# Performance work log

Measured on AMD Instinct MI355X. Metric: run time of the kernel, lower is better.

## Reference

```python
import jax, jax.numpy as jnp
import numpy as np

B, T, C, D, P = 8, 512, 32, 128, 1024
EPS = 1e-5

def setup_inputs() -> dict:
    key = jax.random.key(0)
    ks = jax.random.split(key, 11)
    s = 1.0 / np.sqrt(D)
    inp = {
        'x': jax.random.normal(ks[0], (B, T, C, D), jnp.float32),
        'x_mask': jax.random.randint(ks[1], (B, T, C), 0, 2) == 1,
        'p_mask': jax.random.randint(ks[2], (B, T, C), 0, 2) == 1,
        'pos': jax.random.randint(ks[3], (B, T, C), 0, P),
        'pe': jax.random.normal(ks[4], (P, D // 2, 2), jnp.float32),  # complex rpe as [re, im]
        'imp': jax.random.randint(ks[5], (B, T), 0, C),
        'idx_c': jax.random.randint(ks[6], (B, T, C), 0, C),
        'wq_w': jax.random.normal(ks[7], (D, D), jnp.float32) * s,
        'wq_b': jnp.zeros((D,), jnp.float32),
        'wk_w': jax.random.normal(ks[8], (D, D), jnp.float32) * s,
        'wk_b': jnp.zeros((D,), jnp.float32),
        'wv_w': jax.random.normal(ks[9], (D, D), jnp.float32) * s,
        'wv_b': jnp.zeros((D,), jnp.float32),
        'ls_gamma': 1e-5 * jnp.ones((D,), jnp.float32),
        'ln_gamma': jnp.ones((D,), jnp.float32),
        'ln_beta': jnp.zeros((D,), jnp.float32),
    }
    return inp


def _rotate(z, r):
    # z: (b,t,c,d) real; r: (b,t,c,d/2,2) complex multiplier [re,im]
    b, t, c, d = z.shape
    zr = z.reshape(b, t, c, d // 2, 2)
    re = zr[..., 0] * r[..., 0] - zr[..., 1] * r[..., 1]
    im = zr[..., 0] * r[..., 1] + zr[..., 1] * r[..., 0]
    return jnp.stack([re, im], axis=-1).reshape(b, t, c, d)


def reference(x, x_mask, p_mask, pos, pe, imp, idx_c,
              wq_w, wq_b, wk_w, wk_b, wv_w, wv_b,
              ls_gamma, ln_gamma, ln_beta):
    b, t, c, d = x.shape
    # channel selection gather: where x_mask, use per-token important channel
    imp_rep = jnp.broadcast_to(imp[:, :, None], (b, t, c))
    idx = jnp.where(x_mask, imp_rep, idx_c)            # (b,t,c)
    xg = jnp.take_along_axis(x, idx[..., None], axis=2)  # (b,t,c,d)
    # QKV projections (torch Linear: x @ W.T + b)
    q = xg @ wq_w.T + wq_b
    k = xg @ wk_w.T + wk_b
    v = xg @ wv_w.T + wv_b
    # relative PE complex rotation on q,k
    r = pe[pos]                                        # (b,t,c,d/2,2)
    q = _rotate(q, r)
    k = _rotate(k, r)
    # (b,c,t,d) layout; channel acts as head
    qt = q.transpose(0, 2, 1, 3)
    kt = k.transpose(0, 2, 1, 3)
    vt = v.transpose(0, 2, 1, 3)
    scores = jnp.einsum('bcqd,bckd->bcqk', qt, kt) / jnp.sqrt(jnp.float32(d))
    pm = p_mask.transpose(0, 2, 1)                     # (b,c,t)
    mask = pm[:, :, :, None] | pm[:, :, None, :]       # (b,c,t,t)
    attn = jax.nn.softmax(jnp.where(mask, -jnp.inf, scores), axis=-1)
    attn = jnp.nan_to_num(attn)
    xm = x_mask.transpose(0, 2, 1)                     # (b,c,t)
    weight = jnp.where(xm, 1.0 / t, 1.0)
    out = jnp.einsum('bcmn,bcnd->bmcd', attn * weight[:, :, None, :], vt)  # (b,t,c,d)
    # norm_first=False: LN(x + layer_scale(out))
    y = x + ls_gamma * out
    mu = jnp.mean(y, axis=-1, keepdims=True)
    var = jnp.mean(jnp.square(y - mu), axis=-1, keepdims=True)
    return (y - mu) / jnp.sqrt(var + EPS) * ln_gamma + ln_beta
```

## Files before the change

kernel.cpp:

```cpp
#include <hip/hip_runtime.h>
#include <hip/hip_bf16.h>

#define Bb 8
#define Tt 512
#define Cc 32
#define Dd 128
#define SCALE 0.08838834764831845f
#define SROW 520

typedef unsigned int u32;
typedef __hip_bfloat16 bf16;
typedef __attribute__((ext_vector_type(8))) short short8;
typedef __attribute__((ext_vector_type(4))) short short4v;
typedef __attribute__((ext_vector_type(4))) float floatx4;

__device__ __forceinline__ short f2bf(float f) {
    __hip_bfloat16 h = __float2bfloat16(f);
    return *(short*)&h;
}
__device__ __forceinline__ float bf2f(short s) {
    return __uint_as_float(((u32)(unsigned short)s) << 16);
}

__global__ __launch_bounds__(256)
void k_wconv(const float* __restrict__ wq, const float* __restrict__ wk,
             const float* __restrict__ wv, short* __restrict__ Wb)
{
    int g = blockIdx.x * 256 + threadIdx.x;
    int mat = g >> 14, rem = g & 16383;
    const float* src = (mat == 0) ? wq : (mat == 1) ? wk : wv;
    Wb[g] = f2bf(src[rem]);
}

__global__ __launch_bounds__(256)
void k_qkvm(const float* __restrict__ x, const int* __restrict__ xm,
            const int* __restrict__ pos, const float* __restrict__ pe,
            const int* __restrict__ imp, const int* __restrict__ idxc,
            const short* __restrict__ Wb,
            const float* __restrict__ bq, const float* __restrict__ bk,
            const float* __restrict__ bv,
            short* __restrict__ qb, short* __restrict__ kb, short* __restrict__ vb)
{
    const int R0  = blockIdx.x * 64;
    const int b   = R0 >> 14;
    const int t0  = (R0 >> 5) & 511;
    const int tid = threadIdx.x;
    const int w    = tid >> 6;
    const int lane = tid & 63;
    const int quad = lane >> 4;
    const int m    = lane & 15;

    __shared__ short xg[64 * 136];
    __shared__ short ot[64 * 392];

#pragma unroll
    for (int i = 0; i < 8; ++i) {
        int u   = tid + i * 256;
        int row = u >> 5, seg = u & 31;
        int R   = R0 + row;
        int idx = xm[R] ? imp[R >> 5] : idxc[R];
        float4 v = *(const float4*)(x + ((long)(R >> 5) * Cc + idx) * Dd + seg * 4);
        short4v s = {f2bf(v.x), f2bf(v.y), f2bf(v.z), f2bf(v.w)};
        *(short4v*)&xg[row * 136 + seg * 4] = s;
    }

    short8 wf[6][4];
    float  bias_v[6];
#pragma unroll
    for (int mat = 0; mat < 3; ++mat) {
        const float* bp = (mat == 0) ? bq : (mat == 1) ? bk : bv;
#pragma unroll
        for (int h = 0; h < 2; ++h) {
            int sl = mat * 2 + h;
            int ct = h * 4 + w;
            bias_v[sl] = bp[ct * 16 + m];
#pragma unroll
            for (int kk = 0; kk < 4; ++kk)
                wf[sl][kk] = *(const short8*)(Wb + ((long)mat * 128 + ct * 16 + m) * 128
                                              + kk * 32 + quad * 8);
        }
    }
    __syncthreads();

    for (int rt = 0; rt < 4; ++rt) {
        short8 af[4];
#pragma unroll
        for (int kk = 0; kk < 4; ++kk)
            af[kk] = *(const short8*)&xg[(rt * 16 + m) * 136 + kk * 32 + quad * 8];

        floatx4 acc[6];
#pragma unroll
        for (int sl = 0; sl < 6; ++sl) acc[sl] = (floatx4){0.f, 0.f, 0.f, 0.f};
#pragma unroll
        for (int kk = 0; kk < 4; ++kk)
#pragma unroll
            for (int sl = 0; sl < 6; ++sl)
                acc[sl] = __builtin_amdgcn_mfma_f32_16x16x32_bf16(af[kk], wf[sl][kk], acc[sl], 0, 0, 0);

        int po[4];
#pragma unroll
        for (int r = 0; r < 4; ++r) po[r] = pos[R0 + rt * 16 + quad * 4 + r];

#pragma unroll
        for (int sl = 0; sl < 6; ++sl) {
            int mat = sl >> 1;
            int ct  = (sl & 1) * 4 + w;
            int d   = ct * 16 + m;
#pragma unroll
            for (int r = 0; r < 4; ++r) {
                float v = acc[sl][r] + bias_v[sl];
                float p = __shfl_xor(v, 1, 64);
                if (mat < 2) {
                    const float* rp = pe + ((long)po[r] * (Dd / 2) + (d >> 1)) * 2;
                    float r0 = rp[0], r1 = rp[1];
                    v = (d & 1) ? fmaf(p, r1, v * r0) : fmaf(v, r0, -(p * r1));
                    if (mat == 0) v *= SCALE;
                }
                ot[(rt * 16 + quad * 4 + r) * 392 + mat * 128 + d] = f2bf(v);
            }
        }
    }
    __syncthreads();

    short* const mats[3] = {qb, kb, vb};
#pragma unroll
    for (int mat = 0; mat < 3; ++mat) {
        short* dst = mats[mat];
#pragma unroll
        for (int i = 0; i < 4; ++i) {
            int g = tid + i * 256;
            int n = g >> 4, off = (g & 15) * 8;
            int c = n & 31, tl = n >> 5;
            *(short8*)(dst + (((long)(b * Cc + c) * Tt) + t0 + tl) * Dd + off) =
                *(const short8*)&ot[n * 392 + mat * 128 + off];
        }
    }
}

__global__ __launch_bounds__(256)
void k_vt(const short* __restrict__ vb, const int* __restrict__ xm,
          short* __restrict__ vt)
{
    const int head = blockIdx.y;
    const int b    = head >> 5;
    const int c    = head & 31;
    const int t0   = blockIdx.x * 64;
    const int tid  = threadIdx.x;

    __shared__ short tile[64 * 136];
    __shared__ float wks[64];

    if (tid < 64)
        wks[tid] = xm[((long)b * Tt + t0 + tid) * Cc + c] ? (1.0f / Tt) : 1.0f;

    const short* src = vb + ((long)head * Tt + t0) * Dd;
#pragma unroll
    for (int i = 0; i < 4; ++i) {
        int u = tid + i * 256;
        int row = u >> 4, col = (u & 15) * 8;
        *(short8*)&tile[row * 136 + col] = *(const short8*)(src + row * Dd + col);
    }
    __syncthreads();

    short* dst = vt + (long)head * Dd * Tt + t0;
#pragma unroll
    for (int i = 0; i < 4; ++i) {
        int u = tid + i * 256;
        int d = u >> 3, t8 = (u & 7) * 8;
        short8 v;
#pragma unroll
        for (int j = 0; j < 8; ++j)
            v[j] = f2bf(bf2f(tile[(t8 + j) * 136 + d]) * wks[t8 + j]);
        *(short8*)(dst + (long)d * Tt + t8) = v;
    }
}

__global__ __launch_bounds__(512, 4)
void k_attn(const short* __restrict__ qb, const short* __restrict__ kbp,
            const short* __restrict__ vtp, const float* __restrict__ x,
            const int* __restrict__ pm,
            const float* __restrict__ lsg, const float* __restrict__ lng,
            const float* __restrict__ lnb, float* __restrict__ out)
{
    const int l    = blockIdx.y * 256 + blockIdx.x;
    const int xcd  = l & 7;
    const int sws  = l >> 3;
    const int hh   = sws & 7;
    const int tl   = (sws >> 3) & 7;
    const int gg   = sws >> 6;
    const int head = xcd + ((gg * 8 + hh) << 3);
    const int b    = head >> 5;
    const int c    = head & 31;
    const int qt0  = tl * 64;
    const int tid  = threadIdx.x;
    const int w    = tid >> 6;
    const int lane = tid & 63;
    const int quad = lane >> 4;
    const int m    = lane & 15;
    const int d    = w * 16 + m;

    __shared__ short S[64 * SROW];
    __shared__ u32   pkbits[16];
    __shared__ float rlS[64];
    __shared__ float ps1[8][64];
    __shared__ float ps2[8][64];
    __shared__ float mrs[64][2];

    {
        bool v = pm[((long)b * Tt + tid) * Cc + c] != 0;
        unsigned long long bal = __ballot(v);
        if (lane == 0) {
            pkbits[w * 2]     = (u32)bal;
            pkbits[w * 2 + 1] = (u32)(bal >> 32);
        }
    }

    short8 qf[4][4];
#pragma unroll
    for (int qt = 0; qt < 4; ++qt)
#pragma unroll
        for (int kk = 0; kk < 4; ++kk)
            qf[qt][kk] = *(const short8*)(qb + ((long)head * Tt + qt0 + qt * 16 + m) * Dd
                                          + kk * 32 + quad * 8);
    __syncthreads();

    for (int ch = 0; ch < 4; ++ch) {
        int kt = ch * 128 + w * 16 + m;
        const short* kp = kbp + ((long)head * Tt + kt) * Dd + quad * 8;
        floatx4 sc[4];
#pragma unroll
        for (int qt = 0; qt < 4; ++qt) sc[qt] = (floatx4){0.f, 0.f, 0.f, 0.f};
#pragma unroll
        for (int kk = 0; kk < 4; ++kk) {
            short8 bk = *(const short8*)(kp + kk * 32);
            __builtin_amdgcn_s_setprio(1);
#pragma unroll
            for (int qt = 0; qt < 4; ++qt)
                sc[qt] = __builtin_amdgcn_mfma_f32_16x16x32_bf16(qf[qt][kk], bk, sc[qt], 0, 0, 0);
            __builtin_amdgcn_s_setprio(0);
        }
        bool masked = (pkbits[kt >> 5] >> (kt & 31)) & 1;
#pragma unroll
        for (int qt = 0; qt < 4; ++qt)
#pragma unroll
            for (int r = 0; r < 4; ++r)
                S[(qt * 16 + quad * 4 + r) * SROW + kt] = f2bf(masked ? -1e30f : sc[qt][r]);
    }

    const short* vbase = vtp + (long)head * Dd * Tt + ((long)d) * Tt + quad * 8;
    short8 bvbuf[8];
#pragma unroll
    for (int kv = 0; kv < 8; ++kv)
        bvbuf[kv] = *(const short8*)(vbase + kv * 32);

    float xv[4][4];
#pragma unroll
    for (int qt = 0; qt < 4; ++qt)
#pragma unroll
        for (int r = 0; r < 4; ++r) {
            int row = qt * 16 + quad * 4 + r;
            xv[qt][r] = x[(((long)b * Tt + qt0 + row) * Cc + c) * Dd + d];
        }
    __syncthreads();

    {
        int qi = tid >> 3, part = tid & 7;
        short* rowp = &S[qi * SROW + part * 8];
        short8 sv[8];
#pragma unroll
        for (int j = 0; j < 8; ++j) sv[j] = *(short8*)&rowp[j * 64];
        float mx = -1e30f;
#pragma unroll
        for (int j = 0; j < 8; ++j)
#pragma unroll
            for (int e = 0; e < 8; ++e) mx = fmaxf(mx, bf2f(sv[j][e]));
        mx = fmaxf(mx, __shfl_xor(mx, 1, 64));
        mx = fmaxf(mx, __shfl_xor(mx, 2, 64));
        mx = fmaxf(mx, __shfl_xor(mx, 4, 64));
        float lsum = 0.f;
#pragma unroll
        for (int j = 0; j < 8; ++j)
#pragma unroll
            for (int e = 0; e < 8; ++e) {
                float s = bf2f(sv[j][e]);
                float ex = (s <= -1e29f) ? 0.f : __expf(s - mx);
                sv[j][e] = f2bf(ex);
                lsum += ex;
            }
#pragma unroll
        for (int j = 0; j < 8; ++j) *(short8*)&rowp[j * 64] = sv[j];
        lsum += __shfl_xor(lsum, 1, 64);
        lsum += __shfl_xor(lsum, 2, 64);
        lsum += __shfl_xor(lsum, 4, 64);
        if (part == 0) {
            int t = qt0 + qi;
            bool qmask = (pkbits[t >> 5] >> (t & 31)) & 1;
            rlS[qi] = (lsum > 0.f && !qmask) ? 1.0f / lsum : 0.f;
        }
    }
    __syncthreads();

    floatx4 oa[4];
#pragma unroll
    for (int qt = 0; qt < 4; ++qt) oa[qt] = (floatx4){0.f, 0.f, 0.f, 0.f};

#pragma unroll
    for (int kv = 0; kv < 16; ++kv) {
        short8 bv = bvbuf[kv & 7];
        if (kv < 8) bvbuf[kv] = *(const short8*)(vbase + (kv + 8) * 32);
        __builtin_amdgcn_s_setprio(1);
#pragma unroll
        for (int qt = 0; qt < 4; ++qt) {
            short8 ap = *(const short8*)&S[(qt * 16 + m) * SROW + kv * 32 + quad * 8];
            oa[qt] = __builtin_amdgcn_mfma_f32_16x16x32_bf16(ap, bv, oa[qt], 0, 0, 0);
        }
        __builtin_amdgcn_s_setprio(0);
    }

    const float lg = lsg[d];
    float yv[4][4];
#pragma unroll
    for (int qt = 0; qt < 4; ++qt)
#pragma unroll
        for (int r = 0; r < 4; ++r) {
            int row = qt * 16 + quad * 4 + r;
            float val = oa[qt][r] * rlS[row];
            float y = xv[qt][r] + lg * val;
            yv[qt][r] = y;
        }
#pragma unroll
    for (int qt = 0; qt < 4; ++qt)
#pragma unroll
        for (int r = 0; r < 4; ++r) {
            float a = yv[qt][r], bb = yv[qt][r] * yv[qt][r];
            a += __shfl_xor(a, 1, 64); bb += __shfl_xor(bb, 1, 64);
            a += __shfl_xor(a, 2, 64); bb += __shfl_xor(bb, 2, 64);
            a += __shfl_xor(a, 4, 64); bb += __shfl_xor(bb, 4, 64);
            a += __shfl_xor(a, 8, 64); bb += __shfl_xor(bb, 8, 64);
            if (m == 0) {
                ps1[w][qt * 16 + quad * 4 + r] = a;
                ps2[w][qt * 16 + quad * 4 + r] = bb;
            }
        }
    __syncthreads();
    if (tid < 64) {
        float a = 0.f, bb = 0.f;
#pragma unroll
        for (int wv = 0; wv < 8; ++wv) { a += ps1[wv][tid]; bb += ps2[wv][tid]; }
        float mean = a * (1.0f / Dd);
        float var  = bb * (1.0f / Dd) - mean * mean;
        mrs[tid][0] = mean;
        mrs[tid][1] = rsqrtf(var + 1e-5f);
    }
    __syncthreads();

    const float g = lng[d], be = lnb[d];
#pragma unroll
    for (int qt = 0; qt < 4; ++qt)
#pragma unroll
        for (int r = 0; r < 4; ++r) {
            int row = qt * 16 + quad * 4 + r;
            int t = qt0 + row;
            out[(((long)b * Tt + t) * Cc + c) * Dd + d] =
                (yv[qt][r] - mrs[row][0]) * mrs[row][1] * g + be;
        }
}

extern "C" void kernel_launch(void* const* d_in, const int* in_sizes, int n_in,
                              void* d_out, int out_size, void* d_ws, size_t ws_size,
                              hipStream_t stream) {
    const float* x    = (const float*)d_in[0];
    const int* xmask  = (const int*)d_in[1];
    const int* pmask  = (const int*)d_in[2];
    const int* pos    = (const int*)d_in[3];
    const float* pe   = (const float*)d_in[4];
    const int* imp    = (const int*)d_in[5];
    const int* idxc   = (const int*)d_in[6];
    const float* wq_w = (const float*)d_in[7];
    const float* wq_b = (const float*)d_in[8];
    const float* wk_w = (const float*)d_in[9];
    const float* wk_b = (const float*)d_in[10];
    const float* wv_w = (const float*)d_in[11];
    const float* wv_b = (const float*)d_in[12];
    const float* lsg  = (const float*)d_in[13];
    const float* lng  = (const float*)d_in[14];
    const float* lnb  = (const float*)d_in[15];
    float* out = (float*)d_out;

    size_t n = (size_t)Bb * Cc * Tt * Dd;
    short* qb = (short*)d_ws;
    short* kb = qb + n;
    short* vb = kb + n;
    short* vt = vb + n;
    short* Wb = vt + n;

    k_wconv<<<dim3(3 * Dd * Dd / 256), dim3(256), 0, stream>>>(wq_w, wk_w, wv_w, Wb);
    k_qkvm<<<dim3(Bb * Tt * Cc / 64), dim3(256), 0, stream>>>(
        x, xmask, pos, pe, imp, idxc, Wb, wq_b, wk_b, wv_b, qb, kb, vb);
    k_vt<<<dim3(Tt / 64, Bb * Cc), dim3(256), 0, stream>>>(vb, xmask, vt);
    k_attn<<<dim3(256, 8), dim3(512), 0, stream>>>(
        qb, kb, vt, x, pmask, lsg, lng, lnb, out);
}
```

Before: 346.7 us.

## Swizzle V transpose LDS tile, drop V prefetch and setprio in attention

The V-transpose kernel now XOR-swizzles the 16-byte column groups of its shared tile so the transposed column reads spread across LDS banks instead of conflicting. The attention kernel drops the register-held V prefetch buffer and the early x load. It now loads V directly inside a non-unrolled PV loop and reads x after the PV matmul, and it removes the s_setprio hints. This lowers register pressure, which could help occupancy, but exposes global load latency in the PV loop and the epilogue.

```diff
diff --git a/kernel.cpp b/kernel.cpp
--- a/kernel.cpp
+++ b/kernel.cpp
@@ -157,8 +157,9 @@
 #pragma unroll
     for (int i = 0; i < 4; ++i) {
         int u = tid + i * 256;
-        int row = u >> 4, col = (u & 15) * 8;
-        *(short8*)&tile[row * 136 + col] = *(const short8*)(src + row * Dd + col);
+        int row = u >> 4, col8 = u & 15;
+        int c8 = col8 ^ ((row >> 3) & 7);
+        *(short8*)&tile[row * 136 + c8 * 8] = *(const short8*)(src + row * Dd + col8 * 8);
     }
     __syncthreads();
 
@@ -167,10 +168,12 @@
     for (int i = 0; i < 4; ++i) {
         int u = tid + i * 256;
         int d = u >> 3, t8 = (u & 7) * 8;
+        int key = u & 7;
+        int cs = ((d >> 3) ^ key) * 8 + (d & 7);
         short8 v;
 #pragma unroll
         for (int j = 0; j < 8; ++j)
-            v[j] = f2bf(bf2f(tile[(t8 + j) * 136 + d]) * wks[t8 + j]);
+            v[j] = f2bf(bf2f(tile[(t8 + j) * 136 + cs]) * wks[t8 + j]);
         *(short8*)(dst + (long)d * Tt + t8) = v;
     }
 }
@@ -197,7 +200,6 @@
     const int lane = tid & 63;
     const int quad = lane >> 4;
     const int m    = lane & 15;
-    const int d    = w * 16 + m;
 
     __shared__ short S[64 * SROW];
     __shared__ u32   pkbits[16];
@@ -233,11 +235,9 @@
 #pragma unroll
         for (int kk = 0; kk < 4; ++kk) {
             short8 bk = *(const short8*)(kp + kk * 32);
-            __builtin_amdgcn_s_setprio(1);
 #pragma unroll
             for (int qt = 0; qt < 4; ++qt)
                 sc[qt] = __builtin_amdgcn_mfma_f32_16x16x32_bf16(qf[qt][kk], bk, sc[qt], 0, 0, 0);
-            __builtin_amdgcn_s_setprio(0);
         }
         bool masked = (pkbits[kt >> 5] >> (kt & 31)) & 1;
 #pragma unroll
@@ -246,21 +246,6 @@
             for (int r = 0; r < 4; ++r)
                 S[(qt * 16 + quad * 4 + r) * SROW + kt] = f2bf(masked ? -1e30f : sc[qt][r]);
     }
-
-    const short* vbase = vtp + (long)head * Dd * Tt + ((long)d) * Tt + quad * 8;
-    short8 bvbuf[8];
-#pragma unroll
-    for (int kv = 0; kv < 8; ++kv)
-        bvbuf[kv] = *(const short8*)(vbase + kv * 32);
-
-    float xv[4][4];
-#pragma unroll
-    for (int qt = 0; qt < 4; ++qt)
-#pragma unroll
-        for (int r = 0; r < 4; ++r) {
-            int row = qt * 16 + quad * 4 + r;
-            xv[qt][r] = x[(((long)b * Tt + qt0 + row) * Cc + c) * Dd + d];
-        }
     __syncthreads();
 
     {
@@ -304,35 +289,37 @@
 #pragma unroll
     for (int qt = 0; qt < 4; ++qt) oa[qt] = (floatx4){0.f, 0.f, 0.f, 0.f};
 
-#pragma unroll
+    const short* vbase = vtp + (long)head * Dd * Tt + ((long)(w * 16 + m)) * Tt + quad * 8;
     for (int kv = 0; kv < 16; ++kv) {
-        short8 bv = bvbuf[kv & 7];
-        if (kv < 8) bvbuf[kv] = *(const short8*)(vbase + (kv + 8) * 32);
-        __builtin_amdgcn_s_setprio(1);
+        short8 bv = *(const short8*)(vbase + kv * 32);
 #pragma unroll
         for (int qt = 0; qt < 4; ++qt) {
             short8 ap = *(const short8*)&S[(qt * 16 + m) * SROW + kv * 32 + quad * 8];
             oa[qt] = __builtin_amdgcn_mfma_f32_16x16x32_bf16(ap, bv, oa[qt], 0, 0, 0);
         }
-        __builtin_amdgcn_s_setprio(0);
-    }
-
+    }
+
+    const int d = w * 16 + m;
     const float lg = lsg[d];
     float yv[4][4];
+    float s1[4][4], s2[4][4];
 #pragma unroll
     for (int qt = 0; qt < 4; ++qt)
 #pragma unroll
         for (int r = 0; r < 4; ++r) {
             int row = qt * 16 + quad * 4 + r;
+            int t = qt0 + row;
             float val = oa[qt][r] * rlS[row];
-            float y = xv[qt][r] + lg * val;
+            float y = x[(((long)b * Tt + t) * Cc + c) * Dd + d] + lg * val;
             yv[qt][r] = y;
+            s1[qt][r] = y;
+            s2[qt][r] = y * y;
         }
 #pragma unroll
     for (int qt = 0; qt < 4; ++qt)
 #pragma unroll
         for (int r = 0; r < 4; ++r) {
-            float a = yv[qt][r], bb = yv[qt][r] * yv[qt][r];
+            float a = s1[qt][r], bb = s2[qt][r];
             a += __shfl_xor(a, 1, 64); bb += __shfl_xor(bb, 1, 64);
             a += __shfl_xor(a, 2, 64); bb += __shfl_xor(bb, 2, 64);
             a += __shfl_xor(a, 4, 64); bb += __shfl_xor(bb, 4, 64);
```

Result: faster. 313.5 us (-9.6%).
